# Optimization experiments

Measured on AMD Instinct MI355X. Metric: run time of the kernel, lower is better.

Reference implementation:

```python
import jax, jax.numpy as jnp
import numpy as np

G_OFF = 1e-6
G_ON = 1e-4
K_V = 0.5
BATCH, SIZE_IN, SIZE_OUT = 512, 2048, 2048


def setup_inputs() -> dict:
    key = jax.random.key(0)
    k1, k2 = jax.random.split(key)
    stdv = 1.0 / np.sqrt(SIZE_IN)
    x = jax.random.normal(k1, (BATCH, SIZE_IN), dtype=jnp.float32)
    weights = jax.random.normal(k2, (SIZE_OUT, SIZE_IN), dtype=jnp.float32) * stdv
    bias = jnp.zeros((SIZE_OUT,), dtype=jnp.float32)
    return {"x": x, "weights": weights, "bias": bias}


def reference(x, weights, bias):
    # inputs with bias column of ones: (B, in+1)
    inputs = jnp.concatenate([x, jnp.ones((x.shape[0], 1), dtype=x.dtype)], axis=1)
    # weights_and_bias: (in+1, out)
    wb = jnp.concatenate([weights.T, bias[None, :]], axis=0)

    V = K_V * inputs                               # (B, in+1)
    max_wb = jnp.max(jnp.abs(wb))
    k_G = (G_ON - G_OFF) / max_wb
    k_I = K_V * k_G
    G_eff = k_G * wb
    G_pos = G_OFF + jnp.maximum(G_eff, 0.0)        # (in+1, out)
    G_neg = G_OFF - jnp.minimum(G_eff, 0.0)        # (in+1, out)

    # The torch code builds an interleaved G of shape (in+1, 2*out), computes
    # I_ind = V[:,:,None] * G[None,:,:], sums over the input axis, then takes
    # even - odd columns. That is exactly V @ G_pos - V @ G_neg.
    I_total = V @ G_pos - V @ G_neg                # (B, out)
    return I_total / k_I
```

## Files before the change

### kernel.cpp

```cpp
#include <hip/hip_runtime.h>
#include <hip/hip_bf16.h>


typedef float  float4_t __attribute__((ext_vector_type(4)));
typedef short  short8_t __attribute__((ext_vector_type(8)));
typedef float  floatx4  __attribute__((ext_vector_type(4)));

constexpr int M = 512, N = 2048, K = 2048;
constexpr int BM = 64, BN = 64, BK = 128;
constexpr int NT = K / BK;

constexpr int NX = M * K;
constexpr int NW = N * K;
constexpr int NCONV4 = (NX + NW) / 4;

__global__ __launch_bounds__(256)
void convert_bf16(const float* __restrict__ x, const float* __restrict__ w,
                  unsigned long long* __restrict__ xb,
                  unsigned long long* __restrict__ wb)
{
    const int i = blockIdx.x * 256 + threadIdx.x;
    const bool isx = i < NX / 4;
    const float4_t v = isx ? *(const float4_t*)(x + 4 * (size_t)i)
                           : *(const float4_t*)(w + 4 * (size_t)(i - NX / 4));
    union { __hip_bfloat16 h[4]; unsigned long long u; } p;
    p.h[0] = __float2bfloat16(v.x);
    p.h[1] = __float2bfloat16(v.y);
    p.h[2] = __float2bfloat16(v.z);
    p.h[3] = __float2bfloat16(v.w);
    if (isx) xb[i] = p.u; else wb[i - NX / 4] = p.u;
}

__device__ __forceinline__ void dma16(const void* g, void* l) {
    __builtin_amdgcn_global_load_lds(
        (const __attribute__((address_space(1))) unsigned int*)g,
        (__attribute__((address_space(3))) unsigned int*)l, 16, 0, 0);
}

__global__ __launch_bounds__(512)
void memristor_gemm(const __hip_bfloat16* __restrict__ xb,
                    const __hip_bfloat16* __restrict__ wb,
                    const float* __restrict__ bias, float* __restrict__ out)
{
    __shared__ __align__(16) __hip_bfloat16 As[2][BM][BK];
    __shared__ __align__(16) __hip_bfloat16 Bs[2][BN][BK];

    const int tid  = threadIdx.x;
    const int bn   = blockIdx.x, bm = blockIdx.y;
    const int lane = tid & 63;
    const int wave = tid >> 6;
    const int wsp  = wave & 3;
    const int kp   = wave >> 2;
    const int wm   = (wsp >> 1) * 32;
    const int wn   = (wsp & 1) * 32;
    const int l16  = lane & 15;
    const int quad = lane >> 4;
    const int key  = l16 & 7;

    const int r_in = lane >> 4;
    const int cp   = lane & 15;

    floatx4 acc[2][2];
    #pragma unroll
    for (int i = 0; i < 2; ++i)
        #pragma unroll
        for (int j = 0; j < 2; ++j)
            acc[i][j] = (floatx4){0.f, 0.f, 0.f, 0.f};

    auto stage_dma = [&](int buf, int k0) {
        #pragma unroll
        for (int d = 0; d < 2; ++d) {
            const int rl = wave * 8 + d * 4 + r_in;
            const int cl = cp ^ (rl & 7);
            dma16(xb + ((size_t)(bm * BM + rl) * K + k0 + cl * 8),
                  &As[buf][wave * 8 + d * 4][0]);
            dma16(wb + ((size_t)(bn * BN + rl) * K + k0 + cl * 8),
                  &Bs[buf][wave * 8 + d * 4][0]);
        }
    };

    auto compute = [&](int buf) {
        #pragma unroll
        for (int s = 0; s < 2; ++s) {
            const int ch = (kp * 8 + s * 4 + quad) ^ key;
            short8_t af0 = *(const short8_t*)&As[buf][wm + l16][ch * 8];
            short8_t af1 = *(const short8_t*)&As[buf][wm + 16 + l16][ch * 8];
            short8_t bf0 = *(const short8_t*)&Bs[buf][wn + l16][ch * 8];
            short8_t bf1 = *(const short8_t*)&Bs[buf][wn + 16 + l16][ch * 8];
            acc[0][0] = __builtin_amdgcn_mfma_f32_16x16x32_bf16(af0, bf0, acc[0][0], 0, 0, 0);
            acc[0][1] = __builtin_amdgcn_mfma_f32_16x16x32_bf16(af0, bf1, acc[0][1], 0, 0, 0);
            acc[1][0] = __builtin_amdgcn_mfma_f32_16x16x32_bf16(af1, bf0, acc[1][0], 0, 0, 0);
            acc[1][1] = __builtin_amdgcn_mfma_f32_16x16x32_bf16(af1, bf1, acc[1][1], 0, 0, 0);
        }
    };

    stage_dma(0, 0);
    __syncthreads();

    for (int t = 0; t < NT; ++t) {
        const int cur = t & 1;
        if (t + 1 < NT) stage_dma(cur ^ 1, (t + 1) * BK);
        compute(cur);
        __syncthreads();
    }

    float* scrb = (float*)&As[0][0][0];
    if (kp == 1) {
        #pragma unroll
        for (int i = 0; i < 2; ++i)
            #pragma unroll
            for (int j = 0; j < 2; ++j) {
                float* p = scrb + ((wsp * 32 + j * 16 + l16) * 36 + i * 16 + quad * 4);
                *(floatx4*)p = acc[i][j];
            }
    }
    __syncthreads();
    if (kp == 0) {
        #pragma unroll
        for (int j = 0; j < 2; ++j) {
            const int col = bn * BN + wn + j * 16 + l16;
            const float bv = bias[col];
            #pragma unroll
            for (int i = 0; i < 2; ++i) {
                const floatx4 part = *(const floatx4*)(
                    scrb + ((wsp * 32 + j * 16 + l16) * 36 + i * 16 + quad * 4));
                const int row0 = bm * BM + wm + i * 16 + quad * 4;
                #pragma unroll
                for (int r = 0; r < 4; ++r)
                    out[(size_t)(row0 + r) * N + col] = acc[i][j][r] + part[r] + bv;
            }
        }
    }
}

extern "C" void kernel_launch(void* const* d_in, const int* in_sizes, int n_in,
                              void* d_out, int out_size, void* d_ws, size_t ws_size,
                              hipStream_t stream) {
    const float* x    = (const float*)d_in[0];
    const float* w    = (const float*)d_in[1];
    const float* bias = (const float*)d_in[2];
    float* out = (float*)d_out;

    unsigned long long* xb = (unsigned long long*)d_ws;
    unsigned long long* wb = xb + NX / 4;

    convert_bf16<<<NCONV4 / 256, 256, 0, stream>>>(x, w, xb, wb);

    dim3 grid(N / BN, M / BM);
    memristor_gemm<<<grid, 512, 0, stream>>>(
        (const __hip_bfloat16*)xb, (const __hip_bfloat16*)wb, bias, out);
}
```

Before: 90.63 us.

## Split GEMM along K into four slices with a separate reduce-and-bias kernel

Adds a split-K decomposition: the GEMM grid gains a z dimension of four K-slices, each writing fp32 partial results to workspace. A new reduce kernel sums the four partials and adds the bias. This raises the block count from 256 to 1024 to fill the many CUs on MI355X. The cost is about 16 MB of extra partial-result traffic and one more kernel launch.

```diff
diff --git a/kernel.cpp b/kernel.cpp
--- a/kernel.cpp
+++ b/kernel.cpp
@@ -8,7 +8,9 @@
 
 constexpr int M = 512, N = 2048, K = 2048;
 constexpr int BM = 64, BN = 64, BK = 128;
-constexpr int NT = K / BK;
+constexpr int KSPLIT = 4;
+constexpr int KS  = K / KSPLIT;
+constexpr int NTL = KS / BK;
 
 constexpr int NX = M * K;
 constexpr int NW = N * K;
@@ -40,13 +42,13 @@
 __global__ __launch_bounds__(512)
 void memristor_gemm(const __hip_bfloat16* __restrict__ xb,
                     const __hip_bfloat16* __restrict__ wb,
-                    const float* __restrict__ bias, float* __restrict__ out)
+                    float* __restrict__ part)
 {
     __shared__ __align__(16) __hip_bfloat16 As[2][BM][BK];
     __shared__ __align__(16) __hip_bfloat16 Bs[2][BN][BK];
 
     const int tid  = threadIdx.x;
-    const int bn   = blockIdx.x, bm = blockIdx.y;
+    const int bn   = blockIdx.x, bm = blockIdx.y, bz = blockIdx.z;
     const int lane = tid & 63;
     const int wave = tid >> 6;
     const int wsp  = wave & 3;
@@ -66,6 +68,8 @@
         #pragma unroll
         for (int j = 0; j < 2; ++j)
             acc[i][j] = (floatx4){0.f, 0.f, 0.f, 0.f};
+
+    const int kbase = bz * KS;
 
     auto stage_dma = [&](int buf, int k0) {
         #pragma unroll
@@ -94,12 +98,13 @@
         }
     };
 
-    stage_dma(0, 0);
+    stage_dma(0, kbase);
     __syncthreads();
 
-    for (int t = 0; t < NT; ++t) {
+    #pragma unroll
+    for (int t = 0; t < NTL; ++t) {
         const int cur = t & 1;
-        if (t + 1 < NT) stage_dma(cur ^ 1, (t + 1) * BK);
+        if (t + 1 < NTL) stage_dma(cur ^ 1, kbase + (t + 1) * BK);
         compute(cur);
         __syncthreads();
     }
@@ -116,21 +121,35 @@
     }
     __syncthreads();
     if (kp == 0) {
+        float* pslice = part + (size_t)bz * M * N;
         #pragma unroll
         for (int j = 0; j < 2; ++j) {
             const int col = bn * BN + wn + j * 16 + l16;
-            const float bv = bias[col];
             #pragma unroll
             for (int i = 0; i < 2; ++i) {
-                const floatx4 part = *(const floatx4*)(
+                const floatx4 po = *(const floatx4*)(
                     scrb + ((wsp * 32 + j * 16 + l16) * 36 + i * 16 + quad * 4));
                 const int row0 = bm * BM + wm + i * 16 + quad * 4;
                 #pragma unroll
                 for (int r = 0; r < 4; ++r)
-                    out[(size_t)(row0 + r) * N + col] = acc[i][j][r] + part[r] + bv;
+                    pslice[(size_t)(row0 + r) * N + col] = acc[i][j][r] + po[r];
             }
         }
     }
+}
+
+__global__ __launch_bounds__(256)
+void reduce_bias(const float* __restrict__ part, const float* __restrict__ bias,
+                 float* __restrict__ out)
+{
+    const size_t off = 4 * ((size_t)blockIdx.x * 256 + threadIdx.x);
+    constexpr size_t MN = (size_t)M * N;
+    float4_t s = *(const float4_t*)(part + off);
+    s += *(const float4_t*)(part + MN + off);
+    s += *(const float4_t*)(part + 2 * MN + off);
+    s += *(const float4_t*)(part + 3 * MN + off);
+    s += *(const float4_t*)(bias + (off & (N - 1)));
+    *(float4_t*)(out + off) = s;
 }
 
 extern "C" void kernel_launch(void* const* d_in, const int* in_sizes, int n_in,
@@ -143,10 +162,13 @@
 
     unsigned long long* xb = (unsigned long long*)d_ws;
     unsigned long long* wb = xb + NX / 4;
+    float* part = (float*)((char*)d_ws + (size_t)(NX + NW) * 2);
 
     convert_bf16<<<NCONV4 / 256, 256, 0, stream>>>(x, w, xb, wb);
 
-    dim3 grid(N / BN, M / BM);
+    dim3 grid(N / BN, M / BM, KSPLIT);
     memristor_gemm<<<grid, 512, 0, stream>>>(
-        (const __hip_bfloat16*)xb, (const __hip_bfloat16*)wb, bias, out);
+        (const __hip_bfloat16*)xb, (const __hip_bfloat16*)wb, part);
+
+    reduce_bias<<<(M * N / 4) / 256, 256, 0, stream>>>(part, bias, out);
 }
```

New measurement: 88.27 us. -2.6%, faster.
